# Kernel optimization log

Hardware: AMD Instinct MI355X
Metric: run time of the kernel (lower is better)

The kernel has to match this reference:

```python
import jax, jax.numpy as jnp
import numpy as np

K = 16  # top-k patches kept (module default)

def setup_inputs() -> dict:
    key = jax.random.key(0)
    ks = jax.random.split(key, 5)
    N, D, A, H = 100000, 1024, 128, 256
    x = jax.random.normal(ks[0], (N, D), dtype=jnp.float32)
    Wa1 = jax.random.normal(ks[1], (D, A), dtype=jnp.float32) * (1.0 / np.sqrt(D))
    ba1 = jnp.zeros((A,), dtype=jnp.float32)
    Wa2 = jax.random.normal(ks[2], (A, 1), dtype=jnp.float32) * (1.0 / np.sqrt(A))
    ba2 = jnp.zeros((1,), dtype=jnp.float32)
    Wc1 = jax.random.normal(ks[3], (D, H), dtype=jnp.float32) * (1.0 / np.sqrt(D))
    bc1 = jnp.zeros((H,), dtype=jnp.float32)
    Wc2 = jax.random.normal(ks[4], (H, 1), dtype=jnp.float32) * (1.0 / np.sqrt(H))
    bc2 = jnp.zeros((1,), dtype=jnp.float32)
    return {"x": x, "Wa1": Wa1, "ba1": ba1, "Wa2": Wa2, "ba2": ba2,
            "Wc1": Wc1, "bc1": bc1, "Wc2": Wc2, "bc2": bc2}

def reference(x, Wa1, ba1, Wa2, ba2, Wc1, bc1, Wc2, bc2):
    # attention logits: Linear -> tanh -> Linear, shape [N]
    scores = (jnp.tanh(x @ Wa1 + ba1) @ Wa2 + ba2)[:, 0]
    # top-k selection over patch dim (k < N here)
    top_vals, top_idx = jax.lax.top_k(scores, K)       # [K], [K]
    x_k = x[top_idx]                                    # [K, D] gather
    attn_w = jax.nn.softmax(top_vals)                   # renormalise over k
    slide_embedding = attn_w @ x_k                      # [D] weighted sum
    # classifier MLP (dropout is identity in eval)
    h = jax.nn.relu(slide_embedding @ Wc1 + bc1)
    logit = (h @ Wc2 + bc2)[0]
    # scatter attention weights back into full-length vector
    full_weights = jnp.zeros(x.shape[0], dtype=x.dtype).at[top_idx].set(attn_w)
    return logit, slide_embedding, full_weights, top_idx
```

## Files before the change

kernel.cpp:

```cpp
#include <hip/hip_runtime.h>
#include <cstddef>
#include <cstdint>

#define N_PATCH 100000
#define D_IN    1024
#define A_DIM   128
#define H_DIM   256
#define KTOP    16

#define OUT_LOGIT 0
#define OUT_EMB   1
#define OUT_FW    (1 + D_IN)
#define OUT_TOPI  (OUT_FW + N_PATCH)

#define WS_SCORES 0
#define WS_CANDV  (N_PATCH)
#define WS_CANDI  (N_PATCH + 4096)
#define WS_WPK    (N_PATCH + 2 * 4096 + 64)

#define NB2A  256
#define CHUNK 391

typedef __attribute__((ext_vector_type(8))) short bf8_t;
typedef __attribute__((ext_vector_type(4))) float f4_t;

__global__ __launch_bounds__(256) void k_prepack(
    const float* __restrict__ Wa1, uint4* __restrict__ wpk)
{
    int t = blockIdx.x * 256 + threadIdx.x;
    int lane = t & 63;
    int part = (t >> 6) & 1;
    int nt   = (t >> 7) & 7;
    int ks   = t >> 10;
    int n  = nt * 16 + (lane & 15);
    int k0 = ks * 32 + ((lane >> 4) * 8);
    union { ushort u[8]; uint4 v; } o;
    #pragma unroll
    for (int j = 0; j < 8; ++j) {
        float w = Wa1[(size_t)(k0 + j) * A_DIM + n];
        uint b = __float_as_uint(w);
        if (part == 0) {
            o.u[j] = (ushort)(b >> 16);
        } else {
            float hf = __uint_as_float(b & 0xffff0000u);
            o.u[j] = (ushort)(__float_as_uint(w - hf) >> 16);
        }
    }
    wpk[t] = o.v;
}

__device__ __forceinline__ void split8(const float4& a, const float4& b,
                                       bf8_t& hi, bf8_t& lo)
{
    union { float f[8]; uint u[8]; float4 v4[2]; } X;
    X.v4[0] = a; X.v4[1] = b;
    union { uint u[4]; bf8_t v; } H, L;
    #pragma unroll
    for (int j = 0; j < 4; ++j) {
        uint x0 = X.u[2 * j], x1 = X.u[2 * j + 1];
        H.u[j] = __builtin_amdgcn_perm(x1, x0, 0x07060302);
        float l0 = X.f[2 * j]     - __uint_as_float(x0 & 0xffff0000u);
        float l1 = X.f[2 * j + 1] - __uint_as_float(x1 & 0xffff0000u);
        L.u[j] = __builtin_amdgcn_perm(__float_as_uint(l1), __float_as_uint(l0), 0x07060302);
    }
    hi = H.v; lo = L.v;
}

#define MFMA_BF16 __builtin_amdgcn_mfma_f32_16x16x32_bf16

#define BAR_LDS() do {                                          \
    asm volatile("s_waitcnt lgkmcnt(0)" ::: "memory");          \
    __builtin_amdgcn_s_barrier();                               \
    asm volatile("" ::: "memory");                              \
} while (0)

#define SCORE_STEP(KS, CUR) do {                                               \
    bf8_t ahi0, alo0, ahi1, alo1;                                              \
    split8(A##CUR[0], A##CUR[1], ahi0, alo0);                                  \
    split8(A##CUR[2], A##CUR[3], ahi1, alo1);                                  \
    if ((KS) < 31) {                                                           \
        _Pragma("unroll")                                                      \
        for (int i = 0; i < 4; ++i) sB[(CUR) ^ 1][tid + i * 256] = bpre[i];    \
    }                                                                          \
    {                                                                          \
        const int kp = ((KS) + 2 < 32) ? (KS) + 2 : 31;                        \
        _Pragma("unroll")                                                      \
        for (int i = 0; i < 4; ++i) bpre[i] = wpk[kp * 1024 + tid + i * 256];  \
        A##CUR[0] = *(const float4*)(pa0 + kp * 32);                           \
        A##CUR[1] = *(const float4*)(pa0 + kp * 32 + 4);                       \
        A##CUR[2] = *(const float4*)(pa1 + kp * 32);                           \
        A##CUR[3] = *(const float4*)(pa1 + kp * 32 + 4);                       \
    }                                                                          \
    const bf8_t* sBf = (const bf8_t*)sB[CUR];                                  \
    _Pragma("unroll")                                                          \
    for (int nt = 0; nt < 8; nt += 2) {                                        \
        bf8_t bh0 = sBf[(nt * 2 + 0) * 64 + ln];                               \
        bf8_t bl0 = sBf[(nt * 2 + 1) * 64 + ln];                               \
        bf8_t bh1 = sBf[(nt * 2 + 2) * 64 + ln];                               \
        bf8_t bl1 = sBf[(nt * 2 + 3) * 64 + ln];                               \
        acc[0][nt]     = MFMA_BF16(ahi0, bh0, acc[0][nt],     0, 0, 0);        \
        acc[1][nt]     = MFMA_BF16(ahi1, bh0, acc[1][nt],     0, 0, 0);        \
        acc[0][nt + 1] = MFMA_BF16(ahi0, bh1, acc[0][nt + 1], 0, 0, 0);        \
        acc[1][nt + 1] = MFMA_BF16(ahi1, bh1, acc[1][nt + 1], 0, 0, 0);        \
        acc[0][nt]     = MFMA_BF16(alo0, bh0, acc[0][nt],     0, 0, 0);        \
        acc[1][nt]     = MFMA_BF16(alo1, bh0, acc[1][nt],     0, 0, 0);        \
        acc[0][nt + 1] = MFMA_BF16(alo0, bh1, acc[0][nt + 1], 0, 0, 0);        \
        acc[1][nt + 1] = MFMA_BF16(alo1, bh1, acc[1][nt + 1], 0, 0, 0);        \
        acc[0][nt]     = MFMA_BF16(ahi0, bl0, acc[0][nt],     0, 0, 0);        \
        acc[1][nt]     = MFMA_BF16(ahi1, bl0, acc[1][nt],     0, 0, 0);        \
        acc[0][nt + 1] = MFMA_BF16(ahi0, bl1, acc[0][nt + 1], 0, 0, 0);        \
        acc[1][nt + 1] = MFMA_BF16(ahi1, bl1, acc[1][nt + 1], 0, 0, 0);        \
    }                                                                          \
    BAR_LDS();                                                                 \
} while (0)

__global__ __launch_bounds__(256) void k_scores(
    const float* __restrict__ x, const uint4* __restrict__ wpk,
    const float* __restrict__ ba1, const float* __restrict__ Wa2,
    const float* __restrict__ ba2, float* __restrict__ scores)
{
    __shared__ uint4 sB[2][1024];

    const int tid = threadIdx.x;
    const int ln  = tid & 63;
    const int q   = ln >> 4;
    const int c   = ln & 15;
    const int wv  = tid >> 6;
    const int row0 = blockIdx.x * 128 + wv * 32;

    const int r0 = min(row0 + c,      N_PATCH - 1);
    const int r1 = min(row0 + 16 + c, N_PATCH - 1);
    const float* pa0 = x + (size_t)r0 * D_IN + q * 8;
    const float* pa1 = x + (size_t)r1 * D_IN + q * 8;

    f4_t acc[2][8];
    #pragma unroll
    for (int rt = 0; rt < 2; ++rt)
        #pragma unroll
        for (int nt = 0; nt < 8; ++nt)
            acc[rt][nt] = (f4_t){0.f, 0.f, 0.f, 0.f};

    uint4 bpre[4];
    {
        uint4 b0[4];
        #pragma unroll
        for (int i = 0; i < 4; ++i) b0[i] = wpk[tid + i * 256];
        #pragma unroll
        for (int i = 0; i < 4; ++i) sB[0][tid + i * 256] = b0[i];
    }
    #pragma unroll
    for (int i = 0; i < 4; ++i) bpre[i] = wpk[1024 + tid + i * 256];

    float4 A0[4], A1[4];
    A0[0] = *(const float4*)(pa0);
    A0[1] = *(const float4*)(pa0 + 4);
    A0[2] = *(const float4*)(pa1);
    A0[3] = *(const float4*)(pa1 + 4);
    A1[0] = *(const float4*)(pa0 + 32);
    A1[1] = *(const float4*)(pa0 + 36);
    A1[2] = *(const float4*)(pa1 + 32);
    A1[3] = *(const float4*)(pa1 + 36);

    BAR_LDS();

    for (int ks = 0; ks < 32; ks += 2) {
        SCORE_STEP(ks,     0);
        SCORE_STEP(ks + 1, 1);
    }

    float b1v[8], w2v[8];
    #pragma unroll
    for (int nt = 0; nt < 8; ++nt) {
        b1v[nt] = ba1[nt * 16 + c];
        w2v[nt] = Wa2[nt * 16 + c];
    }
    const float b2 = ba2[0];

    #pragma unroll
    for (int rt = 0; rt < 2; ++rt)
        #pragma unroll
        for (int reg = 0; reg < 4; ++reg) {
            float p = 0.f;
            #pragma unroll
            for (int nt = 0; nt < 8; ++nt)
                p += tanhf(acc[rt][nt][reg] + b1v[nt]) * w2v[nt];
            #pragma unroll
            for (int off = 1; off < 16; off <<= 1)
                p += __shfl_xor(p, off, 64);
            if (c == 0) {
                int row = row0 + rt * 16 + q * 4 + reg;
                if (row < N_PATCH) scores[row] = p + b2;
            }
        }
}

__global__ __launch_bounds__(256) void k_topk_local(
    const float* __restrict__ scores, float* __restrict__ candv,
    int* __restrict__ candi, float* __restrict__ out_fw)
{
    __shared__ float sv[512];
    __shared__ float rv[256];
    __shared__ int   rs[256];
    const int tid  = threadIdx.x;
    const int base = blockIdx.x * CHUNK;

    for (int i = tid; i < 512; i += 256) {
        int g = base + i;
        sv[i] = (i < CHUNK && g < N_PATCH) ? scores[g] : -1e30f;
    }
    for (int i = tid; i < CHUNK; i += 256) {
        int g = base + i;
        if (g < N_PATCH) out_fw[g] = 0.f;
    }
    __syncthreads();

    for (int r = 0; r < KTOP; ++r) {
        float v1 = sv[tid], v2 = sv[tid + 256];
        float bv; int bs;
        if (v2 > v1) { bv = v2; bs = tid + 256; } else { bv = v1; bs = tid; }
        rv[tid] = bv; rs[tid] = bs;
        __syncthreads();
        for (int off = 128; off > 0; off >>= 1) {
            if (tid < off) {
                float ov = rv[tid + off]; int os = rs[tid + off];
                if (ov > rv[tid] || (ov == rv[tid] && os < rs[tid])) {
                    rv[tid] = ov; rs[tid] = os;
                }
            }
            __syncthreads();
        }
        if (tid == 0) {
            int s = rs[0];
            candv[blockIdx.x * KTOP + r] = rv[0];
            candi[blockIdx.x * KTOP + r] = base + s;
            sv[s] = -1e30f;
        }
        __syncthreads();
    }
}

__global__ __launch_bounds__(256) void k_finalize(
    const float* __restrict__ candv, const int* __restrict__ candi,
    const float* __restrict__ x, const float* __restrict__ Wc1,
    const float* __restrict__ bc1, const float* __restrict__ Wc2,
    const float* __restrict__ bc2, float* __restrict__ out)
{
    __shared__ float cv[4096];
    __shared__ int   ci[4096];
    __shared__ float rv[256];
    __shared__ int   rgx[256];
    __shared__ int   rsl[256];
    __shared__ float topv[KTOP];
    __shared__ int   topi[KTOP];
    __shared__ float attn[KTOP];
    __shared__ float semb[D_IN] __attribute__((aligned(16)));
    __shared__ float red[256];
    const int tid = threadIdx.x;

    for (int i = tid; i < 4096; i += 256) { cv[i] = candv[i]; ci[i] = candi[i]; }
    __syncthreads();

    for (int r = 0; r < KTOP; ++r) {
        float bv = -1e38f; int bg = 0x7fffffff; int bs = tid * 16;
        #pragma unroll
        for (int i = 0; i < 16; ++i) {
            int s = tid * 16 + i;
            float v = cv[s]; int g = ci[s];
            if (v > bv || (v == bv && g < bg)) { bv = v; bg = g; bs = s; }
        }
        rv[tid] = bv; rgx[tid] = bg; rsl[tid] = bs;
        __syncthreads();
        for (int off = 128; off > 0; off >>= 1) {
            if (tid < off) {
                if (rv[tid + off] > rv[tid] ||
                    (rv[tid + off] == rv[tid] && rgx[tid + off] < rgx[tid])) {
                    rv[tid] = rv[tid + off]; rgx[tid] = rgx[tid + off]; rsl[tid] = rsl[tid + off];
                }
            }
            __syncthreads();
        }
        if (tid == 0) {
            topv[r] = rv[0]; topi[r] = rgx[0]; cv[rsl[0]] = -1e30f;
        }
        __syncthreads();
    }

    if (tid == 0) {
        float mx = topv[0];
        float s = 0.f;
        for (int k2 = 0; k2 < KTOP; ++k2) {
            float e = expf(topv[k2] - mx);
            attn[k2] = e; s += e;
        }
        float inv = 1.f / s;
        for (int k2 = 0; k2 < KTOP; ++k2) attn[k2] *= inv;
    }
    __syncthreads();

    if (tid < KTOP) {
        out[OUT_TOPI + tid] = (float)topi[tid];
        out[OUT_FW + topi[tid]] = attn[tid];
    }

    float4 e = {0.f, 0.f, 0.f, 0.f};
    #pragma unroll
    for (int k2 = 0; k2 < KTOP; ++k2) {
        const float a = attn[k2];
        const float4 xv = *(const float4*)(x + (size_t)topi[k2] * D_IN + tid * 4);
        e.x = fmaf(a, xv.x, e.x);
        e.y = fmaf(a, xv.y, e.y);
        e.z = fmaf(a, xv.z, e.z);
        e.w = fmaf(a, xv.w, e.w);
    }
    *(float4*)(&semb[tid * 4]) = e;
    out[OUT_EMB + tid * 4 + 0] = e.x;
    out[OUT_EMB + tid * 4 + 1] = e.y;
    out[OUT_EMB + tid * 4 + 2] = e.z;
    out[OUT_EMB + tid * 4 + 3] = e.w;
    __syncthreads();

    float p0 = 0.f, p1 = 0.f, p2 = 0.f, p3 = 0.f;
    #pragma unroll 2
    for (int d = 0; d < D_IN; d += 4) {
        p0 = fmaf(semb[d + 0], Wc1[(size_t)(d + 0) * H_DIM + tid], p0);
        p1 = fmaf(semb[d + 1], Wc1[(size_t)(d + 1) * H_DIM + tid], p1);
        p2 = fmaf(semb[d + 2], Wc1[(size_t)(d + 2) * H_DIM + tid], p2);
        p3 = fmaf(semb[d + 3], Wc1[(size_t)(d + 3) * H_DIM + tid], p3);
    }
    float h = bc1[tid] + ((p0 + p1) + (p2 + p3));
    h = fmaxf(h, 0.f) * Wc2[tid];
    red[tid] = h;
    __syncthreads();
    for (int off = 128; off > 0; off >>= 1) {
        if (tid < off) red[tid] += red[tid + off];
        __syncthreads();
    }
    if (tid == 0) out[OUT_LOGIT] = red[0] + bc2[0];
}

extern "C" void kernel_launch(void* const* d_in, const int* in_sizes, int n_in,
                              void* d_out, int out_size, void* d_ws, size_t ws_size,
                              hipStream_t stream)
{
    const float* x   = (const float*)d_in[0];
    const float* Wa1 = (const float*)d_in[1];
    const float* ba1 = (const float*)d_in[2];
    const float* Wa2 = (const float*)d_in[3];
    const float* ba2 = (const float*)d_in[4];
    const float* Wc1 = (const float*)d_in[5];
    const float* bc1 = (const float*)d_in[6];
    const float* Wc2 = (const float*)d_in[7];
    const float* bc2 = (const float*)d_in[8];
    float* out = (float*)d_out;
    float* ws  = (float*)d_ws;

    float* scores = ws + WS_SCORES;
    float* candv  = ws + WS_CANDV;
    int*   candi  = (int*)(ws + WS_CANDI);
    uint4* wpk    = (uint4*)(ws + WS_WPK);

    dim3 blk(256);
    k_prepack<<<128, blk, 0, stream>>>(Wa1, wpk);
    k_scores<<<(N_PATCH + 127) / 128, blk, 0, stream>>>(x, wpk, ba1, Wa2, ba2, scores);
    k_topk_local<<<NB2A, blk, 0, stream>>>(scores, candv, candi, out + OUT_FW);
    k_finalize<<<1, blk, 0, stream>>>(candv, candi, x, Wc1, bc1, Wc2, bc2, out);
}
```

Baseline: 785.3 us.

## Stagger K-slice order per block and split classifier MLP across blocks

In the score GEMM, each block now starts its K loop at a slice offset set by its block index and wraps around. This spreads simultaneous reads of the packed weights and of x columns across memory channels instead of every block hitting the same slice at once. The single-block classifier matvec over Wc1 (1 MB) is moved into a 16-block partial-product kernel plus a small reduction kernel, adding two launches in exchange for more parallel memory bandwidth on that tail stage.

```diff
diff --git a/kernel.cpp b/kernel.cpp
--- a/kernel.cpp
+++ b/kernel.cpp
@@ -16,7 +16,9 @@
 #define WS_SCORES 0
 #define WS_CANDV  (N_PATCH)
 #define WS_CANDI  (N_PATCH + 4096)
-#define WS_WPK    (N_PATCH + 2 * 4096 + 64)
+#define WS_EMB    (N_PATCH + 2 * 4096)
+#define WS_HPART  (WS_EMB + D_IN)
+#define WS_WPK    (WS_HPART + 16 * H_DIM)
 
 #define NB2A  256
 #define CHUNK 391
@@ -83,13 +85,13 @@
         for (int i = 0; i < 4; ++i) sB[(CUR) ^ 1][tid + i * 256] = bpre[i];    \
     }                                                                          \
     {                                                                          \
-        const int kp = ((KS) + 2 < 32) ? (KS) + 2 : 31;                        \
+        const int kact = (s0 + (KS) + 2) & 31;    \
         _Pragma("unroll")                                                      \
-        for (int i = 0; i < 4; ++i) bpre[i] = wpk[kp * 1024 + tid + i * 256];  \
-        A##CUR[0] = *(const float4*)(pa0 + kp * 32);                           \
-        A##CUR[1] = *(const float4*)(pa0 + kp * 32 + 4);                       \
-        A##CUR[2] = *(const float4*)(pa1 + kp * 32);                           \
-        A##CUR[3] = *(const float4*)(pa1 + kp * 32 + 4);                       \
+        for (int i = 0; i < 4; ++i) bpre[i] = wpk[kact * 1024 + tid + i * 256];\
+        A##CUR[0] = *(const float4*)(pa0 + kact * 32);                         \
+        A##CUR[1] = *(const float4*)(pa0 + kact * 32 + 4);                     \
+        A##CUR[2] = *(const float4*)(pa1 + kact * 32);                         \
+        A##CUR[3] = *(const float4*)(pa1 + kact * 32 + 4);                     \
     }                                                                          \
     const bf8_t* sBf = (const bf8_t*)sB[CUR];                                  \
     _Pragma("unroll")                                                          \
@@ -127,6 +129,7 @@
     const int c   = ln & 15;
     const int wv  = tid >> 6;
     const int row0 = blockIdx.x * 128 + wv * 32;
+    const int s0   = blockIdx.x & 31;
 
     const int r0 = min(row0 + c,      N_PATCH - 1);
     const int r1 = min(row0 + 16 + c, N_PATCH - 1);
@@ -144,22 +147,29 @@
     {
         uint4 b0[4];
         #pragma unroll
-        for (int i = 0; i < 4; ++i) b0[i] = wpk[tid + i * 256];
+        for (int i = 0; i < 4; ++i) b0[i] = wpk[s0 * 1024 + tid + i * 256];
         #pragma unroll
         for (int i = 0; i < 4; ++i) sB[0][tid + i * 256] = b0[i];
     }
-    #pragma unroll
-    for (int i = 0; i < 4; ++i) bpre[i] = wpk[1024 + tid + i * 256];
+    {
+        const int k1 = (s0 + 1) & 31;
+        #pragma unroll
+        for (int i = 0; i < 4; ++i) bpre[i] = wpk[k1 * 1024 + tid + i * 256];
+    }
 
     float4 A0[4], A1[4];
-    A0[0] = *(const float4*)(pa0);
-    A0[1] = *(const float4*)(pa0 + 4);
-    A0[2] = *(const float4*)(pa1);
-    A0[3] = *(const float4*)(pa1 + 4);
-    A1[0] = *(const float4*)(pa0 + 32);
-    A1[1] = *(const float4*)(pa0 + 36);
-    A1[2] = *(const float4*)(pa1 + 32);
-    A1[3] = *(const float4*)(pa1 + 36);
+    {
+        const int ka = s0;
+        const int kb = (s0 + 1) & 31;
+        A0[0] = *(const float4*)(pa0 + ka * 32);
+        A0[1] = *(const float4*)(pa0 + ka * 32 + 4);
+        A0[2] = *(const float4*)(pa1 + ka * 32);
+        A0[3] = *(const float4*)(pa1 + ka * 32 + 4);
+        A1[0] = *(const float4*)(pa0 + kb * 32);
+        A1[1] = *(const float4*)(pa0 + kb * 32 + 4);
+        A1[2] = *(const float4*)(pa1 + kb * 32);
+        A1[3] = *(const float4*)(pa1 + kb * 32 + 4);
+    }
 
     BAR_LDS();
 
@@ -241,9 +251,8 @@
 
 __global__ __launch_bounds__(256) void k_finalize(
     const float* __restrict__ candv, const int* __restrict__ candi,
-    const float* __restrict__ x, const float* __restrict__ Wc1,
-    const float* __restrict__ bc1, const float* __restrict__ Wc2,
-    const float* __restrict__ bc2, float* __restrict__ out)
+    const float* __restrict__ x, float* __restrict__ out,
+    float* __restrict__ emb)
 {
     __shared__ float cv[4096];
     __shared__ int   ci[4096];
@@ -253,8 +262,6 @@
     __shared__ float topv[KTOP];
     __shared__ int   topi[KTOP];
     __shared__ float attn[KTOP];
-    __shared__ float semb[D_IN] __attribute__((aligned(16)));
-    __shared__ float red[256];
     const int tid = threadIdx.x;
 
     for (int i = tid; i < 4096; i += 256) { cv[i] = candv[i]; ci[i] = candi[i]; }
@@ -312,22 +319,38 @@
         e.z = fmaf(a, xv.z, e.z);
         e.w = fmaf(a, xv.w, e.w);
     }
-    *(float4*)(&semb[tid * 4]) = e;
     out[OUT_EMB + tid * 4 + 0] = e.x;
     out[OUT_EMB + tid * 4 + 1] = e.y;
     out[OUT_EMB + tid * 4 + 2] = e.z;
     out[OUT_EMB + tid * 4 + 3] = e.w;
-    __syncthreads();
-
-    float p0 = 0.f, p1 = 0.f, p2 = 0.f, p3 = 0.f;
-    #pragma unroll 2
-    for (int d = 0; d < D_IN; d += 4) {
-        p0 = fmaf(semb[d + 0], Wc1[(size_t)(d + 0) * H_DIM + tid], p0);
-        p1 = fmaf(semb[d + 1], Wc1[(size_t)(d + 1) * H_DIM + tid], p1);
-        p2 = fmaf(semb[d + 2], Wc1[(size_t)(d + 2) * H_DIM + tid], p2);
-        p3 = fmaf(semb[d + 3], Wc1[(size_t)(d + 3) * H_DIM + tid], p3);
-    }
-    float h = bc1[tid] + ((p0 + p1) + (p2 + p3));
+    *(float4*)(emb + tid * 4) = e;
+}
+
+__global__ __launch_bounds__(256) void k_mlp1(
+    const float* __restrict__ emb, const float* __restrict__ Wc1,
+    float* __restrict__ hpart)
+{
+    __shared__ float se[64];
+    const int b = blockIdx.x, tid = threadIdx.x;
+    if (tid < 64) se[tid] = emb[b * 64 + tid];
+    __syncthreads();
+    float p = 0.f;
+    #pragma unroll 8
+    for (int d = 0; d < 64; ++d)
+        p = fmaf(se[d], Wc1[(size_t)(b * 64 + d) * H_DIM + tid], p);
+    hpart[b * H_DIM + tid] = p;
+}
+
+__global__ __launch_bounds__(256) void k_logit(
+    const float* __restrict__ hpart, const float* __restrict__ bc1,
+    const float* __restrict__ Wc2, const float* __restrict__ bc2,
+    float* __restrict__ out)
+{
+    __shared__ float red[256];
+    const int tid = threadIdx.x;
+    float h = bc1[tid];
+    #pragma unroll
+    for (int i = 0; i < 16; ++i) h += hpart[i * H_DIM + tid];
     h = fmaxf(h, 0.f) * Wc2[tid];
     red[tid] = h;
     __syncthreads();
@@ -357,11 +380,15 @@
     float* scores = ws + WS_SCORES;
     float* candv  = ws + WS_CANDV;
     int*   candi  = (int*)(ws + WS_CANDI);
+    float* emb    = ws + WS_EMB;
+    float* hpart  = ws + WS_HPART;
     uint4* wpk    = (uint4*)(ws + WS_WPK);
 
     dim3 blk(256);
     k_prepack<<<128, blk, 0, stream>>>(Wa1, wpk);
     k_scores<<<(N_PATCH + 127) / 128, blk, 0, stream>>>(x, wpk, ba1, Wa2, ba2, scores);
     k_topk_local<<<NB2A, blk, 0, stream>>>(scores, candv, candi, out + OUT_FW);
-    k_finalize<<<1, blk, 0, stream>>>(candv, candi, x, Wc1, bc1, Wc2, bc2, out);
-}
+    k_finalize<<<1, blk, 0, stream>>>(candv, candi, x, out, emb);
+    k_mlp1<<<16, blk, 0, stream>>>(emb, Wc1, hpart);
+    k_logit<<<1, blk, 0, stream>>>(hpart, bc1, Wc2, bc2, out);
+}
```

Measured after the change: 718.3 us. -8.5%, faster.
